# Optimization experiments

Measured on AMD Instinct MI355X. Metric: run time of the kernel, lower is better.

The kernel has to match this reference:

```python
import jax, jax.numpy as jnp
import numpy as np

# config (mirrors init_kwargs)
R = 1.0           # ball-query radius
K = 32            # ball-query neighbors
SPATIAL_STRIDE = 4
TKS = 3           # temporal kernel size (odd)
TPAD = (1, 1)     # replicate temporal padding
HEADS = 8
DIM_HEAD = 64
DIM = 512
MLP = 2048
DEPTH = 2
LN_EPS = 1e-5


def fps(xyz, m):
    # CUDA-style furthest point sampling, starts at index 0. xyz: [N,3] -> [m] int32
    N = xyz.shape[0]
    def body(carry, _):
        dists, last = carry
        d = jnp.sum((xyz - xyz[last]) ** 2, axis=-1)
        dists = jnp.minimum(dists, d)
        nxt = jnp.argmax(dists).astype(jnp.int32)
        return (dists, nxt), nxt
    init = (jnp.full((N,), 1e10, xyz.dtype), jnp.int32(0))
    _, idxs = jax.lax.scan(body, init, None, length=m - 1)
    return jnp.concatenate([jnp.zeros((1,), jnp.int32), idxs])


def ball_query(neighbor_xyz, anchor_xyz):
    # first K neighbor indices within radius R (pad with first found, 0 if none)
    N = neighbor_xyz.shape[0]
    d2 = jnp.sum((anchor_xyz[:, None, :] - neighbor_xyz[None, :, :]) ** 2, -1)  # [M,N]
    cand = jnp.where(d2 < R * R, jnp.arange(N, dtype=jnp.int32)[None, :], N)
    firstk = jnp.sort(cand, axis=-1)[:, :K]
    first = firstk[:, :1]
    idx = jnp.where(firstk >= N, first, firstk)
    return jnp.where(idx >= N, 0, idx).astype(jnp.int32)


def layer_norm(x, g, b):
    mu = jnp.mean(x, -1, keepdims=True)
    var = jnp.var(x, -1, keepdims=True)
    return (x - mu) * jax.lax.rsqrt(var + LN_EPS) * g + b


def p4dconv(xyzs, Wd):
    # tube embedding: FPS anchors + ball-query grouping + 1x1 conv on (dx,dy,dz,dt)
    B, T, N, _ = xyzs.shape
    pad = jnp.concatenate([xyzs[:, :1]] * TPAD[0] + [xyzs] + [xyzs[:, -1:]] * TPAD[1], axis=1)
    Lp = pad.shape[1]
    m = N // SPATIAL_STRIDE
    half = TKS // 2
    new_xyzs, new_feats = [], []
    for t in range(half, Lp - half, 1):  # temporal_stride = 1
        frame = pad[:, t]                                  # [B,N,3]
        aidx = jax.vmap(lambda x: fps(x, m))(frame)        # [B,m]
        anchor = jax.vmap(lambda f, ix: f[ix])(frame, aidx)  # [B,m,3]
        feats_t = []
        for i in range(t - half, t + half + 1):
            nb = pad[:, i]                                 # [B,N,3]
            idx = jax.vmap(ball_query)(nb, anchor)         # [B,m,K]
            grouped = jax.vmap(lambda n, ix: n[ix])(nb, idx)  # [B,m,K,3]
            disp = grouped - anchor[:, :, None, :]
            tdisp = jnp.full((B, m, K, 1), float(i - t), disp.dtype)
            d4 = jnp.concatenate([disp, tdisp], -1)        # [B,m,K,4]
            f = jnp.einsum('bmkf,cf->bmkc', d4, Wd)        # 1x1 conv, no bias/BN/act
            feats_t.append(jnp.max(f, axis=2))             # spatial max pool
        new_feats.append(jnp.max(jnp.stack(feats_t, 1), axis=1))  # temporal max pool
        new_xyzs.append(anchor)
    return jnp.stack(new_xyzs, 1), jnp.stack(new_feats, 1)  # [B,L,m,3], [B,L,m,C]


def attention(xyzs, feats, Wqkv, Wsp, Wout, bout, g, b):
    B, L, n, C = feats.shape
    M = L * n
    x = layer_norm(feats, g, b)
    qkv = jnp.einsum('blnc,ec->blne', x, Wqkv).reshape(B, M, 3, HEADS, DIM_HEAD)
    q, k, v = [jnp.transpose(qkv[:, :, j], (0, 2, 1, 3)) for j in range(3)]  # [B,h,M,d]
    dots = jnp.einsum('bhid,bhjd->bhij', q, k) * (DIM_HEAD ** -0.5)
    attn = jax.nn.softmax(dots, axis=-1)
    out_v = jnp.einsum('bhij,bhjd->bhid', attn, v)
    xyz_f = xyzs.reshape(B, M, 3)
    delta = xyz_f[:, None, :, :] - xyz_f[:, :, None, :]      # [B,i,j,3] = xyz_j - xyz_i
    wdelta = jnp.einsum('bhij,bijc->bhic', attn, delta)      # attn-weighted displacement
    disp_f = jnp.einsum('bhic,dc->bhid', wdelta, Wsp)        # spatial_op Linear(3->d)
    out = out_v + disp_f
    out = jnp.transpose(out, (0, 2, 1, 3)).reshape(B, M, HEADS * DIM_HEAD)
    out = jax.nn.gelu(out @ Wout.T + bout, approximate=False)
    return out.reshape(B, L, n, C) + feats


def feed_forward(x, g, b, W1, b1, W2, b2):
    h = layer_norm(x, g, b)
    h = jax.nn.gelu(h @ W1.T + b1, approximate=False)
    return h @ W2.T + b2 + x


def setup_inputs() -> dict:
    key = jax.random.key(0)
    ks = jax.random.split(key, 12)
    s = 0.02
    inner = HEADS * DIM_HEAD
    return {
        'xyzs': jax.random.normal(ks[0], (2, 4, 1024, 3), jnp.float32),
        'Wd': jax.random.normal(ks[1], (DIM, 4), jnp.float32) * s,
        'Wqkv': jax.random.normal(ks[2], (DEPTH, 3 * inner, DIM), jnp.float32) * s,
        'Wsp': jax.random.normal(ks[3], (DEPTH, DIM_HEAD, 3), jnp.float32) * s,
        'Wout': jax.random.normal(ks[4], (DEPTH, DIM, inner), jnp.float32) * s,
        'bout': jnp.zeros((DEPTH, DIM), jnp.float32),
        'ln1_g': jnp.ones((DEPTH, DIM), jnp.float32),
        'ln1_b': jnp.zeros((DEPTH, DIM), jnp.float32),
        'Wff1': jax.random.normal(ks[5], (DEPTH, MLP, DIM), jnp.float32) * s,
        'bff1': jnp.zeros((DEPTH, MLP), jnp.float32),
        'Wff2': jax.random.normal(ks[6], (DEPTH, DIM, MLP), jnp.float32) * s,
        'bff2': jnp.zeros((DEPTH, DIM), jnp.float32),
        'ln2_g': jnp.ones((DEPTH, DIM), jnp.float32),
        'ln2_b': jnp.zeros((DEPTH, DIM), jnp.float32),
    }


def reference(xyzs, Wd, Wqkv, Wsp, Wout, bout, ln1_g, ln1_b, Wff1, bff1, Wff2, bff2, ln2_g, ln2_b):
    new_xyzs, feats = p4dconv(xyzs, Wd)   # [B,L,m,3], [B,L,m,DIM]
    feats = jax.nn.relu(feats)            # emb_relu after tube embedding
    for i in range(DEPTH):
        feats = attention(new_xyzs, feats, Wqkv[i], Wsp[i], Wout[i], bout[i], ln1_g[i], ln1_b[i])
        feats = feed_forward(feats, ln2_g[i], ln2_b[i], Wff1[i], bff1[i], Wff2[i], bff2[i])
    return feats
```

## Files before the change

kernel.cpp:

```cpp
#include <hip/hip_runtime.h>
#include <math.h>
#include <stdint.h>


typedef __bf16 bf16_t;
typedef __bf16 bf16x8 __attribute__((ext_vector_type(8)));
typedef __bf16 bf16x4 __attribute__((ext_vector_type(4)));
typedef float f32x4 __attribute__((ext_vector_type(4)));

__device__ __forceinline__ void async16(const bf16_t* g, bf16_t* l) {
  __builtin_amdgcn_global_load_lds(
      (const __attribute__((address_space(1))) void*)g,
      (__attribute__((address_space(3))) void*)l, 16, 0, 0);
}

__device__ __forceinline__ float wave_max_dpp(float v) {
  int a = __float_as_int(v);
  int t;
  t = __builtin_amdgcn_update_dpp(a, a, 0x111, 0xf, 0xf, false);
  a = __float_as_int(fmaxf(__int_as_float(a), __int_as_float(t)));
  t = __builtin_amdgcn_update_dpp(a, a, 0x112, 0xf, 0xf, false);
  a = __float_as_int(fmaxf(__int_as_float(a), __int_as_float(t)));
  t = __builtin_amdgcn_update_dpp(a, a, 0x114, 0xf, 0xf, false);
  a = __float_as_int(fmaxf(__int_as_float(a), __int_as_float(t)));
  t = __builtin_amdgcn_update_dpp(a, a, 0x118, 0xf, 0xf, false);
  a = __float_as_int(fmaxf(__int_as_float(a), __int_as_float(t)));
  t = __builtin_amdgcn_update_dpp(a, a, 0x142, 0xf, 0xf, false);
  a = __float_as_int(fmaxf(__int_as_float(a), __int_as_float(t)));
  t = __builtin_amdgcn_update_dpp(a, a, 0x143, 0xf, 0xf, false);
  a = __float_as_int(fmaxf(__int_as_float(a), __int_as_float(t)));
  return __int_as_float(a);
}

__global__ __launch_bounds__(256) void fps_kernel(const float* __restrict__ xyzs,
                                                  float* __restrict__ anchors) {
  int bid = blockIdx.x;
  int to = bid & 3, b = bid >> 2;
  const float* fr = xyzs + (size_t)(b * 4 + to) * 1024 * 3;
  float* an = anchors + (size_t)(b * 4 + to) * 256 * 3;
  __shared__ __align__(16) float4 sp[1024];
  __shared__ __align__(16) unsigned long long keys[4];
  int tid = threadIdx.x;
  int w = tid >> 6, lane = tid & 63;
  float px[4], py[4], pz[4], dist[4];
#pragma unroll
  for (int r = 0; r < 4; ++r) {
    int i = r * 256 + tid;
    float x = fr[i * 3 + 0], y = fr[i * 3 + 1], z = fr[i * 3 + 2];
    px[r] = x; py[r] = y; pz[r] = z; dist[r] = 1e10f;
    sp[i] = make_float4(x, y, z, 0.0f);
  }
  __syncthreads();
  float4 c = sp[0];
  if (tid == 0) { an[0] = c.x; an[1] = c.y; an[2] = c.z; }
  for (int s = 1; s < 256; ++s) {
#pragma unroll
    for (int r = 0; r < 4; ++r) {
      float dx = px[r] - c.x, dy = py[r] - c.y, dz = pz[r] - c.z;
      float d = fmaf(dx, dx, fmaf(dy, dy, dz * dz));
      dist[r] = fminf(dist[r], d);
    }
    float m01 = fmaxf(dist[0], dist[1]), m23 = fmaxf(dist[2], dist[3]);
    float mloc = fmaxf(m01, m23);
    float wmax = wave_max_dpp(mloc);
    float smax = __int_as_float(__builtin_amdgcn_readlane(__float_as_int(wmax), 63));
    unsigned int cidx = 0xFFFFFFFFu;
#pragma unroll
    for (int r = 3; r >= 0; --r) {
      unsigned long long m = __ballot(dist[r] == smax);
      unsigned int tz = (unsigned int)__builtin_ctzll(m | 0x8000000000000000ull);
      unsigned int cand = (unsigned int)(r * 256 + w * 64) + tz;
      cidx = m ? cand : cidx;
    }
    unsigned long long key =
        ((unsigned long long)__float_as_uint(smax) << 32) |
        (unsigned long long)(~cidx);
    if (lane == 0) keys[w] = key;
    __syncthreads();
    unsigned long long k0 = keys[0], k1 = keys[1];
    unsigned long long k2 = keys[2], k3 = keys[3];
    unsigned long long ka = k0 > k1 ? k0 : k1;
    unsigned long long kb = k2 > k3 ? k2 : k3;
    unsigned long long kk = ka > kb ? ka : kb;
    unsigned int bi = ~(unsigned int)(kk & 0xFFFFFFFFull);
    c = sp[bi];
    if (tid == 0) { an[s * 3 + 0] = c.x; an[s * 3 + 1] = c.y; an[s * 3 + 2] = c.z; }
    __syncthreads();
  }
}

__global__ __launch_bounds__(192) void conv_kernel(
    const float* __restrict__ xyzs, const float* __restrict__ anchors,
    const float* __restrict__ Wd, float* __restrict__ feats) {
  int bid = blockIdx.x;
  int j = bid & 255, to = (bid >> 8) & 3, b = bid >> 10;
  __shared__ float disp[96][4];
  __shared__ int idxbuf[3][32];
  const float* an = anchors + (size_t)((b * 4 + to) * 256 + j) * 3;
  float ax = an[0], ay = an[1], az = an[2];
  int w = threadIdx.x >> 6, lane = threadIdx.x & 63;
  int src = to + w - 1; src = src < 0 ? 0 : (src > 3 ? 3 : src);
  const float* nb = xyzs + (size_t)(b * 4 + src) * 1024 * 3;
  int cnt = 0;
  for (int ch = 0; ch < 16; ++ch) {
    if (cnt >= 32) break;
    int i = ch * 64 + lane;
    float dx = ax - nb[i * 3], dy = ay - nb[i * 3 + 1], dz = az - nb[i * 3 + 2];
    float d2 = dx * dx + dy * dy + dz * dz;
    bool in = d2 < 1.0f;
    unsigned long long mask = __ballot(in);
    if (in) {
      int pos = cnt + (int)__popcll(mask & ((1ull << lane) - 1ull));
      if (pos < 32) idxbuf[w][pos] = i;
    }
    cnt += (int)__popcll(mask);
  }
  if (cnt > 32) cnt = 32;
  if (lane >= cnt && lane < 32) idxbuf[w][lane] = (cnt > 0) ? idxbuf[w][0] : 0;
  if (lane < 32) {
    int ni = idxbuf[w][lane];
    int row = w * 32 + lane;
    disp[row][0] = nb[ni * 3 + 0] - ax;
    disp[row][1] = nb[ni * 3 + 1] - ay;
    disp[row][2] = nb[ni * 3 + 2] - az;
    disp[row][3] = (float)(w - 1);
  }
  __syncthreads();
  float* fout = feats + ((size_t)(b * 1024) + to * 256 + j) * 512;
  for (int c = threadIdx.x; c < 512; c += 192) {
    const float* wr = Wd + c * 4;
    float w0 = wr[0], w1 = wr[1], w2 = wr[2], w3 = wr[3];
    float mx = -1e30f;
#pragma unroll 8
    for (int nn = 0; nn < 96; ++nn) {
      float v = disp[nn][0] * w0 + disp[nn][1] * w1 + disp[nn][2] * w2 + disp[nn][3] * w3;
      mx = fmaxf(mx, v);
    }
    fout[c] = fmaxf(mx, 0.0f);
  }
}

__global__ __launch_bounds__(256) void cvt_all_kernel(
    const float* __restrict__ s0, bf16_t* __restrict__ d0,
    const float* __restrict__ s1, bf16_t* __restrict__ d1,
    const float* __restrict__ s2, bf16_t* __restrict__ d2,
    const float* __restrict__ s3, bf16_t* __restrict__ d3) {
  int idx = blockIdx.x * 256 + threadIdx.x;
  const float* s; bf16_t* d; int off;
  if (idx < 393216) { s = s0; d = d0; off = idx; }
  else if (idx < 524288) { s = s1; d = d1; off = idx - 393216; }
  else if (idx < 1048576) { s = s2; d = d2; off = idx - 524288; }
  else { s = s3; d = d3; off = idx - 1048576; }
  float4 v = ((const float4*)s)[off];
  bf16x4 o = {(bf16_t)v.x, (bf16_t)v.y, (bf16_t)v.z, (bf16_t)v.w};
  ((bf16x4*)d)[off] = o;
}

__global__ __launch_bounds__(256) void ln_kernel(
    const float* __restrict__ x, const float* __restrict__ g,
    const float* __restrict__ bt, bf16_t* __restrict__ y) {
  int row = blockIdx.x;
  int tid = threadIdx.x;
  const float* xr = x + (size_t)row * 512;
  float v0 = xr[tid], v1 = xr[tid + 256];
  float s = v0 + v1;
#pragma unroll
  for (int off = 32; off >= 1; off >>= 1) s += __shfl_xor(s, off, 64);
  __shared__ float red1[4], red2[4];
  int w = tid >> 6, lane = tid & 63;
  if (lane == 0) red1[w] = s;
  __syncthreads();
  float mu = (red1[0] + red1[1] + red1[2] + red1[3]) * (1.0f / 512.0f);
  float d0 = v0 - mu, d1 = v1 - mu;
  float q = d0 * d0 + d1 * d1;
#pragma unroll
  for (int off = 32; off >= 1; off >>= 1) q += __shfl_xor(q, off, 64);
  if (lane == 0) red2[w] = q;
  __syncthreads();
  float var = (red2[0] + red2[1] + red2[2] + red2[3]) * (1.0f / 512.0f);
  float rs = rsqrtf(var + 1e-5f);
  bf16_t* yr = y + (size_t)row * 512;
  yr[tid] = (bf16_t)(d0 * rs * g[tid] + bt[tid]);
  yr[tid + 256] = (bf16_t)(d1 * rs * g[tid + 256] + bt[tid + 256]);
}

template <int BM, int BN, bool GELU, bool BIAS, bool RES, bool OUTBF>
__global__ __launch_bounds__(256) void gemm_bf16(
    const bf16_t* __restrict__ A, const bf16_t* __restrict__ W,
    const float* __restrict__ bias, const float* __restrict__ res,
    void* __restrict__ Cout, int Mn, int Nn, int Kn) {
  constexpr int BK = 32;
  constexpr int WM = BM / 2, WN = BN / 2;
  constexpr int MT = WM / 16, NT = WN / 16;
  constexpr int APW = (BM / 16) / 4;
  constexpr int BPW = (BN / 16) / 4;
  __shared__ __align__(16) bf16_t As[BM * BK];
  __shared__ __align__(16) bf16_t Bs[BN * BK];
  int tid = threadIdx.x;
  int w = tid >> 6, lane = tid & 63;
  int wr = w >> 1, wc = w & 1;
  int m0 = blockIdx.y * BM, n0 = blockIdx.x * BN;
  int lrow = lane >> 2;
  int lk8 = (lane & 3) * 8;
  f32x4 acc[MT][NT] = {};

  const int a_fo = (wr * WM + (lane & 15)) * BK + (lane >> 4) * 8;
  const int b_fo = (wc * WN + (lane & 15)) * BK + (lane >> 4) * 8;

  for (int k0 = 0; k0 < Kn; k0 += BK) {
    __syncthreads();
#pragma unroll
    for (int i = 0; i < APW; ++i) {
      int g = w + i * 4;
      const bf16_t* gp = A + ((size_t)(m0 + g * 16 + lrow) * Kn + k0 + lk8);
      async16(gp, As + g * 16 * BK);
    }
#pragma unroll
    for (int i = 0; i < BPW; ++i) {
      int g = w + i * 4;
      const bf16_t* gp = W + ((size_t)(n0 + g * 16 + lrow) * Kn + k0 + lk8);
      async16(gp, Bs + g * 16 * BK);
    }
    __syncthreads();
    bf16x8 aF[MT], bF[NT];
#pragma unroll
    for (int mt = 0; mt < MT; ++mt)
      aF[mt] = *(const bf16x8*)&As[a_fo + mt * 16 * BK];
#pragma unroll
    for (int nt = 0; nt < NT; ++nt)
      bF[nt] = *(const bf16x8*)&Bs[b_fo + nt * 16 * BK];
#pragma unroll
    for (int mt = 0; mt < MT; ++mt)
#pragma unroll
      for (int nt = 0; nt < NT; ++nt)
        acc[mt][nt] = __builtin_amdgcn_mfma_f32_16x16x32_bf16(
            aF[mt], bF[nt], acc[mt][nt], 0, 0, 0);
  }
  int rbase = (lane >> 4) * 4;
  int col_l = lane & 15;
#pragma unroll
  for (int mt = 0; mt < MT; ++mt) {
#pragma unroll
    for (int reg = 0; reg < 4; ++reg) {
      int r = m0 + wr * WM + mt * 16 + rbase + reg;
      size_t roff = (size_t)r * Nn;
#pragma unroll
      for (int nt = 0; nt < NT; ++nt) {
        int c = n0 + wc * WN + nt * 16 + col_l;
        float v = acc[mt][nt][reg];
        if (BIAS) v += bias[c];
        if (GELU) v = v * 0.5f * (1.0f + erff(v * 0.7071067811865475f));
        if (RES) v += res[roff + c];
        if (OUTBF) ((bf16_t*)Cout)[roff + c] = (bf16_t)v;
        else ((float*)Cout)[roff + c] = v;
      }
    }
  }
}

__global__ __launch_bounds__(256) void attn_kernel(
    const bf16_t* __restrict__ qkv, const float* __restrict__ xyzf,
    const float* __restrict__ Wsp, bf16_t* __restrict__ outp) {
  int bid = blockIdx.x;
  int qt = bid & 15, h = (bid >> 4) & 7, b = bid >> 7;
  int tid = threadIdx.x;
  int w = tid >> 6, lane = tid & 63;
  int l15 = lane & 15, quad = lane >> 4;

  __shared__ __align__(16) bf16_t Kb[64 * 64];
  __shared__ __align__(16) bf16_t Vt[64 * 72];
  __shared__ __align__(16) bf16_t Ps[4][16 * 72];
  __shared__ __align__(16) float4 Xs[64];

  const size_t tokbase = (size_t)b * 1024;
  int qbase = qt * 64 + w * 16;

  bf16x8 aQ[2];
  {
    const bf16_t* qp = qkv + (tokbase + qbase + l15) * 1536 + h * 64 + quad * 8;
    aQ[0] = *(const bf16x8*)(qp);
    aQ[1] = *(const bf16x8*)(qp + 32);
  }

  f32x4 oacc[4] = {};
  float lr[4] = {}, pxr[4] = {}, pyr[4] = {}, pzr[4] = {};

  for (int ch = 0; ch < 16; ++ch) {
    int j0 = ch * 64;
    __syncthreads();
    {
      int r0 = tid >> 3, seg = tid & 7;
      const bf16_t* g0 = qkv + (tokbase + j0 + r0) * 1536 + 512 + h * 64 + seg * 8;
      async16(g0, Kb + tid * 8);
      const bf16_t* g1 = qkv + (tokbase + j0 + 32 + r0) * 1536 + 512 + h * 64 + seg * 8;
      async16(g1, Kb + 2048 + tid * 8);
    }
#pragma unroll
    for (int t = 0; t < 4; ++t) {
      int task = t * 256 + tid;
      int rp = task >> 5, c2 = task & 31;
      const uint32_t* vsrc = (const uint32_t*)(qkv + (tokbase + j0 + 2 * rp) * 1536 +
                                               1024 + h * 64 + 2 * c2);
      uint32_t a = vsrc[0];
      uint32_t bq = vsrc[768];
      uint32_t wlo = (a & 0xffffu) | (bq << 16);
      uint32_t whi = (a >> 16) | (bq & 0xffff0000u);
      uint32_t* vd = (uint32_t*)Vt;
      vd[c2 * 72 + rp] = wlo;
      vd[c2 * 72 + 36 + rp] = whi;
    }
    if (tid < 64) {
      const float* xp = xyzf + (tokbase + j0 + tid) * 3;
      Xs[tid] = make_float4(xp[0], xp[1], xp[2], 0.0f);
    }
    __syncthreads();
    f32x4 sacc[4] = {};
#pragma unroll
    for (int ks = 0; ks < 2; ++ks)
#pragma unroll
      for (int nt = 0; nt < 4; ++nt) {
        bf16x8 bK = *(const bf16x8*)&Kb[(nt * 16 + l15) * 64 + ks * 32 + quad * 8];
        sacc[nt] = __builtin_amdgcn_mfma_f32_16x16x32_bf16(aQ[ks], bK, sacc[nt], 0, 0, 0);
      }
#pragma unroll
    for (int nt = 0; nt < 4; ++nt) {
      float4 xk = Xs[nt * 16 + l15];
#pragma unroll
      for (int reg = 0; reg < 4; ++reg) {
        float p = __expf(sacc[nt][reg] * 0.125f);
        bf16_t pb = (bf16_t)p;
        float pf = (float)pb;
        Ps[w][(quad * 4 + reg) * 72 + nt * 16 + l15] = pb;
        lr[reg] += pf;
        pxr[reg] = fmaf(pf, xk.x, pxr[reg]);
        pyr[reg] = fmaf(pf, xk.y, pyr[reg]);
        pzr[reg] = fmaf(pf, xk.z, pzr[reg]);
      }
    }
    bf16x8 aP[2];
    aP[0] = *(const bf16x8*)&Ps[w][l15 * 72 + quad * 8];
    aP[1] = *(const bf16x8*)&Ps[w][l15 * 72 + 32 + quad * 8];
#pragma unroll
    for (int ks = 0; ks < 2; ++ks)
#pragma unroll
      for (int ct = 0; ct < 4; ++ct) {
        bf16x8 bV = *(const bf16x8*)&Vt[(ct * 16 + l15) * 72 + ks * 32 + quad * 8];
        oacc[ct] = __builtin_amdgcn_mfma_f32_16x16x32_bf16(aP[ks], bV, oacc[ct], 0, 0, 0);
      }
  }
#pragma unroll
  for (int reg = 0; reg < 4; ++reg) {
#pragma unroll
    for (int off = 1; off <= 8; off <<= 1) {
      lr[reg] += __shfl_xor(lr[reg], off, 64);
      pxr[reg] += __shfl_xor(pxr[reg], off, 64);
      pyr[reg] += __shfl_xor(pyr[reg], off, 64);
      pzr[reg] += __shfl_xor(pzr[reg], off, 64);
    }
  }
#pragma unroll
  for (int reg = 0; reg < 4; ++reg) {
    size_t tok = tokbase + qbase + quad * 4 + reg;
    float inv = 1.0f / lr[reg];
    const float* xqp = xyzf + tok * 3;
    float wd0 = pxr[reg] * inv - xqp[0];
    float wd1 = pyr[reg] * inv - xqp[1];
    float wd2 = pzr[reg] * inv - xqp[2];
#pragma unroll
    for (int ct = 0; ct < 4; ++ct) {
      int c = ct * 16 + l15;
      const float* wr = Wsp + c * 3;
      float dv = wd0 * wr[0] + wd1 * wr[1] + wd2 * wr[2];
      outp[tok * 512 + h * 64 + c] = (bf16_t)(oacc[ct][reg] * inv + dv);
    }
  }
}

extern "C" void kernel_launch(void* const* d_in, const int* in_sizes, int n_in,
                              void* d_out, int out_size, void* d_ws, size_t ws_size,
                              hipStream_t stream) {
  const float* xyzs = (const float*)d_in[0];
  const float* Wd   = (const float*)d_in[1];
  const float* Wqkv = (const float*)d_in[2];
  const float* Wsp  = (const float*)d_in[3];
  const float* Wout = (const float*)d_in[4];
  const float* bout = (const float*)d_in[5];
  const float* ln1g = (const float*)d_in[6];
  const float* ln1b = (const float*)d_in[7];
  const float* Wff1 = (const float*)d_in[8];
  const float* bff1 = (const float*)d_in[9];
  const float* Wff2 = (const float*)d_in[10];
  const float* bff2 = (const float*)d_in[11];
  const float* ln2g = (const float*)d_in[12];
  const float* ln2b = (const float*)d_in[13];
  float* out = (float*)d_out;

  float* ws = (float*)d_ws;
  float* anchors = ws;
  float* featsA  = ws + 8192;
  float* featsB  = featsA + 1048576;
  float* big     = featsB + 1048576;
  bf16_t* bigb   = (bf16_t*)big;
  bf16_t* xlnb   = (bf16_t*)(big + 3145728);
  bf16_t* attob  = xlnb + 1048576;
  bf16_t* wq_b   = attob + 1048576;
  bf16_t* wo_b   = wq_b + 1572864;
  bf16_t* w1_b   = wo_b + 524288;
  bf16_t* w2_b   = w1_b + 2097152;

  fps_kernel<<<8, 256, 0, stream>>>(xyzs, anchors);
  cvt_all_kernel<<<6144, 256, 0, stream>>>(Wqkv, wq_b, Wout, wo_b,
                                           Wff1, w1_b, Wff2, w2_b);
  conv_kernel<<<2048, 192, 0, stream>>>(xyzs, anchors, Wd, featsA);

  for (int dep = 0; dep < 2; ++dep) {
    ln_kernel<<<2048, 256, 0, stream>>>(featsA, ln1g + dep * 512, ln1b + dep * 512, xlnb);
    gemm_bf16<128, 128, false, false, false, true><<<dim3(12, 16), 256, 0, stream>>>(
        xlnb, wq_b + (size_t)dep * 786432, nullptr, nullptr, bigb, 2048, 1536, 512);
    attn_kernel<<<256, 256, 0, stream>>>(bigb, anchors, Wsp + dep * 192, attob);
    gemm_bf16<64, 64, true, true, true, false><<<dim3(8, 32), 256, 0, stream>>>(
        attob, wo_b + (size_t)dep * 262144, bout + dep * 512, featsA, featsB,
        2048, 512, 512);
    ln_kernel<<<2048, 256, 0, stream>>>(featsB, ln2g + dep * 512, ln2b + dep * 512, xlnb);
    gemm_bf16<128, 128, true, true, false, true><<<dim3(16, 16), 256, 0, stream>>>(
        xlnb, w1_b + (size_t)dep * 1048576, bff1 + dep * 2048, nullptr, bigb,
        2048, 2048, 512);
    float* dst = (dep == 1) ? out : featsA;
    gemm_bf16<64, 64, false, true, true, false><<<dim3(8, 32), 256, 0, stream>>>(
        bigb, w2_b + (size_t)dep * 1048576, bff2 + dep * 512, featsB, dst,
        2048, 512, 2048);
  }
}
```

Measured before the change: 479.4 us.

## Drop a barrier per FPS step with double-buffered keys and DPP key reduction

The furthest-point-sampling kernel now runs 512 threads (8 waves), each handling 2 points instead of 4, which shortens the per-thread serial work in each of the 255 sequential steps. The per-wave argmax keys go into a double-buffered shared array indexed by step parity, so the second __syncthreads per iteration can be removed. The cross-wave max is now a 3-step DPP 64-bit reduction across lanes instead of four scalar shared-memory reads and compares. The trade-offs are more waves joining each barrier and extra DPP instructions for the 64-bit compare.

Result: no change. 474.0 us (-1.1%).

```diff
diff --git a/kernel.cpp b/kernel.cpp
--- a/kernel.cpp
+++ b/kernel.cpp
@@ -32,20 +32,31 @@
   return __int_as_float(a);
 }
 
-__global__ __launch_bounds__(256) void fps_kernel(const float* __restrict__ xyzs,
+template <int CTRL>
+__device__ __forceinline__ unsigned long long dpp_max_u64(unsigned long long kv) {
+  uint32_t lo = (uint32_t)kv, hi = (uint32_t)(kv >> 32);
+  uint32_t lo2 =
+      (uint32_t)__builtin_amdgcn_update_dpp((int)lo, (int)lo, CTRL, 0xf, 0xf, false);
+  uint32_t hi2 =
+      (uint32_t)__builtin_amdgcn_update_dpp((int)hi, (int)hi, CTRL, 0xf, 0xf, false);
+  unsigned long long other = ((unsigned long long)hi2 << 32) | lo2;
+  return other > kv ? other : kv;
+}
+
+__global__ __launch_bounds__(512) void fps_kernel(const float* __restrict__ xyzs,
                                                   float* __restrict__ anchors) {
   int bid = blockIdx.x;
   int to = bid & 3, b = bid >> 2;
   const float* fr = xyzs + (size_t)(b * 4 + to) * 1024 * 3;
   float* an = anchors + (size_t)(b * 4 + to) * 256 * 3;
   __shared__ __align__(16) float4 sp[1024];
-  __shared__ __align__(16) unsigned long long keys[4];
+  __shared__ __align__(16) unsigned long long keys[2][8];
   int tid = threadIdx.x;
   int w = tid >> 6, lane = tid & 63;
-  float px[4], py[4], pz[4], dist[4];
-#pragma unroll
-  for (int r = 0; r < 4; ++r) {
-    int i = r * 256 + tid;
+  float px[2], py[2], pz[2], dist[2];
+#pragma unroll
+  for (int r = 0; r < 2; ++r) {
+    int i = r * 512 + tid;
     float x = fr[i * 3 + 0], y = fr[i * 3 + 1], z = fr[i * 3 + 2];
     px[r] = x; py[r] = y; pz[r] = z; dist[r] = 1e10f;
     sp[i] = make_float4(x, y, z, 0.0f);
@@ -54,38 +65,36 @@
   float4 c = sp[0];
   if (tid == 0) { an[0] = c.x; an[1] = c.y; an[2] = c.z; }
   for (int s = 1; s < 256; ++s) {
-#pragma unroll
-    for (int r = 0; r < 4; ++r) {
+    int par = s & 1;
+#pragma unroll
+    for (int r = 0; r < 2; ++r) {
       float dx = px[r] - c.x, dy = py[r] - c.y, dz = pz[r] - c.z;
       float d = fmaf(dx, dx, fmaf(dy, dy, dz * dz));
       dist[r] = fminf(dist[r], d);
     }
-    float m01 = fmaxf(dist[0], dist[1]), m23 = fmaxf(dist[2], dist[3]);
-    float mloc = fmaxf(m01, m23);
+    float mloc = fmaxf(dist[0], dist[1]);
     float wmax = wave_max_dpp(mloc);
     float smax = __int_as_float(__builtin_amdgcn_readlane(__float_as_int(wmax), 63));
     unsigned int cidx = 0xFFFFFFFFu;
 #pragma unroll
-    for (int r = 3; r >= 0; --r) {
+    for (int r = 1; r >= 0; --r) {
       unsigned long long m = __ballot(dist[r] == smax);
       unsigned int tz = (unsigned int)__builtin_ctzll(m | 0x8000000000000000ull);
-      unsigned int cand = (unsigned int)(r * 256 + w * 64) + tz;
+      unsigned int cand = (unsigned int)(r * 512 + w * 64) + tz;
       cidx = m ? cand : cidx;
     }
     unsigned long long key =
         ((unsigned long long)__float_as_uint(smax) << 32) |
         (unsigned long long)(~cidx);
-    if (lane == 0) keys[w] = key;
+    if (lane == 0) keys[par][w] = key;
     __syncthreads();
-    unsigned long long k0 = keys[0], k1 = keys[1];
-    unsigned long long k2 = keys[2], k3 = keys[3];
-    unsigned long long ka = k0 > k1 ? k0 : k1;
-    unsigned long long kb = k2 > k3 ? k2 : k3;
-    unsigned long long kk = ka > kb ? ka : kb;
-    unsigned int bi = ~(unsigned int)(kk & 0xFFFFFFFFull);
+    unsigned long long kv = keys[par][lane & 7];
+    kv = dpp_max_u64<0xB1>(kv);
+    kv = dpp_max_u64<0x4E>(kv);
+    kv = dpp_max_u64<0x124>(kv);
+    unsigned int bi = ~(unsigned int)(kv & 0xFFFFFFFFull);
     c = sp[bi];
     if (tid == 0) { an[s * 3 + 0] = c.x; an[s * 3 + 1] = c.y; an[s * 3 + 2] = c.z; }
-    __syncthreads();
   }
 }
 
@@ -408,7 +417,7 @@
   bf16_t* w1_b   = wo_b + 524288;
   bf16_t* w2_b   = w1_b + 2097152;
 
-  fps_kernel<<<8, 256, 0, stream>>>(xyzs, anchors);
+  fps_kernel<<<8, 512, 0, stream>>>(xyzs, anchors);
   cvt_all_kernel<<<6144, 256, 0, stream>>>(Wqkv, wq_b, Wout, wo_b,
                                            Wff1, w1_b, Wff2, w2_b);
   conv_kernel<<<2048, 192, 0, stream>>>(xyzs, anchors, Wd, featsA);
```
